# Kernel tuning notes

Measured on AMD Instinct MI355X. Metric: run time of the kernel, lower is better.

## Reference

```python
import jax, jax.numpy as jnp
import numpy as np

CUTOFF = 5.0
N_ATOMS, N_EDGES, D, R = 100000, 1600000, 64, 20


def setup_inputs() -> dict:
    key = jax.random.key(0)
    ks = jax.random.split(key, 12)
    ve = jax.random.normal(ks[0], (N_ATOMS, D, 3), dtype=jnp.float32)
    se = jax.random.normal(ks[1], (N_ATOMS, D), dtype=jnp.float32)
    dirs = jax.random.normal(ks[2], (N_EDGES, 3), dtype=jnp.float32)
    dirs = dirs / jnp.linalg.norm(dirs, axis=-1, keepdims=True)
    dist = jax.random.uniform(ks[3], (N_EDGES,), minval=0.5, maxval=CUTOFF, dtype=jnp.float32)
    nv = dirs * dist[:, None]  # neighbour_vectors with norm in (0.5, cutoff)
    central = jax.random.randint(ks[4], (N_EDGES,), 0, N_ATOMS)
    neigh = jax.random.randint(ks[5], (N_EDGES,), 0, N_ATOMS)
    # Bessel frequencies n*pi/cutoff (learnable in graph-pes)
    freqs = (jnp.arange(1, R + 1, dtype=jnp.float32) * np.pi / CUTOFF)
    W_filter = jax.random.normal(ks[6], (R, 3 * D), dtype=jnp.float32) / np.sqrt(R)
    b_filter = jnp.zeros((3 * D,), dtype=jnp.float32)
    W1 = jax.random.normal(ks[7], (D, D), dtype=jnp.float32) / np.sqrt(D)
    b1 = jnp.zeros((D,), dtype=jnp.float32)
    W2 = jax.random.normal(ks[8], (D, 3 * D), dtype=jnp.float32) / np.sqrt(D)
    b2 = jnp.zeros((3 * D,), dtype=jnp.float32)
    return {
        'vector_embeddings': ve, 'scalar_embeddings': se, 'neighbour_vectors': nv,
        'central_atoms': central, 'neighbours': neigh,
        'freqs': freqs, 'W_filter': W_filter, 'b_filter': b_filter,
        'W1': W1, 'b1': b1, 'W2': W2, 'b2': b2,
    }


def _envelope(d):
    # polynomial envelope, p = 6
    u = d / CUTOFF
    env = 1.0 - 28.0 * u**6 + 48.0 * u**7 - 21.0 * u**8
    return jnp.where(d < CUTOFF, env, 0.0)


def reference(vector_embeddings, scalar_embeddings, neighbour_vectors,
              central_atoms, neighbours, freqs, W_filter, b_filter,
              W1, b1, W2, b2):
    d = jnp.linalg.norm(neighbour_vectors, axis=-1)                 # [E]
    unit = neighbour_vectors / d[:, None]                           # [E, 3]
    # Bessel radial basis: sqrt(2/c) * sin(f_n d) / d
    bessel = np.sqrt(2.0 / CUTOFF) * jnp.sin(freqs[None, :] * d[:, None]) / d[:, None]  # [E, R]
    filt = (bessel @ W_filter + b_filter) * _envelope(d)[:, None]   # [E, 3D]
    # phi: MLP [D, D, 3D] with SiLU between layers
    h = jax.nn.silu(scalar_embeddings @ W1 + b1) @ W2 + b2          # [N, 3D]
    x_ij = filt * h[central_atoms]                                  # [E, 3D]
    a, b, c = jnp.split(x_ij, 3, axis=-1)                           # each [E, D]
    n = scalar_embeddings.shape[0]
    delta_s = jax.ops.segment_sum(a, neighbours, num_segments=n)    # [N, D]
    v_ij = b[:, :, None] * unit[:, None, :] + c[:, :, None] * vector_embeddings[neighbours]  # [E, D, 3]
    delta_v = jax.ops.segment_sum(v_ij, neighbours, num_segments=n)  # [N, D, 3]
    return (delta_v, delta_s)
```

## Files before the change

kernel.cpp:

```cpp
#include <hip/hip_runtime.h>
#include <math.h>

#define DCH 64
#define TD 192
#define RR 20
#define FCUT 5.0f

typedef __attribute__((ext_vector_type(8))) short short8;
typedef __attribute__((ext_vector_type(4))) float f32x4;
typedef __attribute__((ext_vector_type(2))) unsigned int u32x2;

__device__ __forceinline__ unsigned short f2bf(float f) {
    unsigned int u = __float_as_uint(f);
    u += 0x7FFFu + ((u >> 16) & 1u);
    return (unsigned short)(u >> 16);
}
__device__ __forceinline__ float bflo(unsigned int u) {
    return __uint_as_float(u << 16);
}
__device__ __forceinline__ float bfhi(unsigned int u) {
    return __uint_as_float(u & 0xFFFF0000u);
}

__global__ __launch_bounds__(256, 2) void mlp_mfma_kernel(
    const float* __restrict__ se,
    const float* __restrict__ W1, const float* __restrict__ b1,
    const float* __restrict__ W2, const float* __restrict__ b2,
    unsigned short* __restrict__ h2, int N)
{
    const int wid  = threadIdx.x >> 6;
    const int lane = threadIdx.x & 63;
    const int g    = lane >> 4;
    const int c    = lane & 15;

    __shared__ float hmid[4][16][68];
    __shared__ unsigned short hstage[4][16][196];

    short8 W1f[4][2];
    float  b1t[4];
    #pragma unroll
    for (int t = 0; t < 4; ++t) {
        #pragma unroll
        for (int kh = 0; kh < 2; ++kh)
            #pragma unroll
            for (int j = 0; j < 8; ++j) {
                int k = kh * 32 + 8 * g + j;
                W1f[t][kh][j] = (short)f2bf(W1[k * DCH + 16 * t + c]);
            }
        b1t[t] = b1[16 * t + c];
    }
    short8 W2f[12][2];
    float  b2t[12];
    #pragma unroll
    for (int t = 0; t < 12; ++t) {
        #pragma unroll
        for (int kh = 0; kh < 2; ++kh)
            #pragma unroll
            for (int j = 0; j < 8; ++j) {
                int k = kh * 32 + 8 * g + j;
                W2f[t][kh][j] = (short)f2bf(W2[k * TD + 16 * t + c]);
            }
        b2t[t] = b2[16 * t + c];
    }

    for (int base = blockIdx.x * 64; base < N; base += gridDim.x * 64) {
        const int arow = base + wid * 16;
        const int atom = arow + c;
        const bool va  = atom < N;

        const float* sp = se + (size_t)(va ? atom : 0) * DCH;
        short8 A0, A1;
        #pragma unroll
        for (int kh = 0; kh < 2; ++kh) {
            f32x4 q0 = va ? __builtin_nontemporal_load((const f32x4*)(sp + kh*32 + 8*g))
                          : (f32x4){0.f,0.f,0.f,0.f};
            f32x4 q1 = va ? __builtin_nontemporal_load((const f32x4*)(sp + kh*32 + 8*g + 4))
                          : (f32x4){0.f,0.f,0.f,0.f};
            short8& A = kh ? A1 : A0;
            A[0] = (short)f2bf(q0[0]); A[1] = (short)f2bf(q0[1]);
            A[2] = (short)f2bf(q0[2]); A[3] = (short)f2bf(q0[3]);
            A[4] = (short)f2bf(q1[0]); A[5] = (short)f2bf(q1[1]);
            A[6] = (short)f2bf(q1[2]); A[7] = (short)f2bf(q1[3]);
        }

        #pragma unroll
        for (int t = 0; t < 4; ++t) {
            f32x4 C = {0.f, 0.f, 0.f, 0.f};
            C = __builtin_amdgcn_mfma_f32_16x16x32_bf16(A0, W1f[t][0], C, 0, 0, 0);
            C = __builtin_amdgcn_mfma_f32_16x16x32_bf16(A1, W1f[t][1], C, 0, 0, 0);
            #pragma unroll
            for (int reg = 0; reg < 4; ++reg) {
                float x = C[reg] + b1t[t];
                float s = x / (1.0f + __expf(-x));
                hmid[wid][4 * g + reg][16 * t + c] = s;
            }
        }
        __syncthreads();

        short8 B0, B1;
        #pragma unroll
        for (int kh = 0; kh < 2; ++kh) {
            const float* hp = &hmid[wid][c][kh * 32 + 8 * g];
            f32x4 q0 = *(const f32x4*)(hp);
            f32x4 q1 = *(const f32x4*)(hp + 4);
            short8& A = kh ? B1 : B0;
            A[0] = (short)f2bf(q0[0]); A[1] = (short)f2bf(q0[1]);
            A[2] = (short)f2bf(q0[2]); A[3] = (short)f2bf(q0[3]);
            A[4] = (short)f2bf(q1[0]); A[5] = (short)f2bf(q1[1]);
            A[6] = (short)f2bf(q1[2]); A[7] = (short)f2bf(q1[3]);
        }

        #pragma unroll
        for (int t = 0; t < 12; ++t) {
            f32x4 C = {0.f, 0.f, 0.f, 0.f};
            C = __builtin_amdgcn_mfma_f32_16x16x32_bf16(B0, W2f[t][0], C, 0, 0, 0);
            C = __builtin_amdgcn_mfma_f32_16x16x32_bf16(B1, W2f[t][1], C, 0, 0, 0);
            #pragma unroll
            for (int reg = 0; reg < 4; ++reg)
                hstage[wid][4 * g + reg][c * 12 + t] = f2bf(C[reg] + b2t[t]);
        }
        __syncthreads();

        if (lane < 48) {
            #pragma unroll
            for (int i = 0; i < 16; ++i) {
                int a2 = arow + i;
                if (a2 < N)
                    *(u32x2*)((char*)h2 + (size_t)a2 * 384 + lane * 8) =
                        *(const u32x2*)(&hstage[wid][i][lane * 4]);
            }
        }
    }
}

__global__ void hist_kernel(const int* __restrict__ neigh,
                            int* __restrict__ counts, int* __restrict__ pos, int E)
{
    int stride = gridDim.x * blockDim.x;
    for (int e = blockIdx.x * blockDim.x + threadIdx.x; e < E; e += stride) {
        int p = atomicAdd(&counts[neigh[e]], 1);
        __builtin_nontemporal_store(p, &pos[e]);
    }
}

__global__ __launch_bounds__(256) void scan1_kernel(
    const int* __restrict__ counts, int* __restrict__ starts,
    int* __restrict__ bsums, int N)
{
    int tid = threadIdx.x;
    int gid = blockIdx.x * 256 + tid;
    int v = (gid < N) ? counts[gid] : 0;
    int lane = tid & 63, wid = tid >> 6;
    int x = v;
    #pragma unroll
    for (int off = 1; off < 64; off <<= 1) {
        int y = __shfl_up(x, off, 64);
        if (lane >= off) x += y;
    }
    __shared__ int wsum[4];
    if (lane == 63) wsum[wid] = x;
    __syncthreads();
    int add = 0;
    for (int w = 0; w < wid; ++w) add += wsum[w];
    int incl = x + add;
    if (gid < N) starts[gid] = incl - v;
    if (tid == 255) bsums[blockIdx.x] = incl;
}

__global__ __launch_bounds__(512) void scan2_kernel(int* __restrict__ bsums, int M)
{
    int tid = threadIdx.x;
    int v = (tid < M) ? bsums[tid] : 0;
    int lane = tid & 63, wid = tid >> 6;
    int x = v;
    #pragma unroll
    for (int off = 1; off < 64; off <<= 1) {
        int y = __shfl_up(x, off, 64);
        if (lane >= off) x += y;
    }
    __shared__ int wsum[8];
    if (lane == 63) wsum[wid] = x;
    __syncthreads();
    int add = 0;
    for (int w = 0; w < wid; ++w) add += wsum[w];
    int incl = x + add;
    if (tid < M) bsums[tid] = incl - v;
}

__global__ __launch_bounds__(256) void scan3_kernel(
    int* __restrict__ starts, const int* __restrict__ bsums, int N)
{
    int gid = blockIdx.x * 256 + threadIdx.x;
    if (gid < N) starts[gid] += bsums[blockIdx.x];
}

__global__ void fill_kernel(const float* __restrict__ nv, const int* __restrict__ central,
                            const int* __restrict__ neigh, const int* __restrict__ starts,
                            const int* __restrict__ pos, f32x4* __restrict__ payload, int E)
{
    int stride = gridDim.x * blockDim.x;
    for (int e = blockIdx.x * blockDim.x + threadIdx.x; e < E; e += stride) {
        int slot = starts[neigh[e]] + pos[e];
        f32x4 pay;
        pay[0] = __builtin_nontemporal_load(&nv[(size_t)e*3+0]);
        pay[1] = __builtin_nontemporal_load(&nv[(size_t)e*3+1]);
        pay[2] = __builtin_nontemporal_load(&nv[(size_t)e*3+2]);
        pay[3] = __int_as_float(central[e]);
        __builtin_nontemporal_store(pay, &payload[slot]);
    }
}

__global__ __launch_bounds__(256) void gather_kernel(
    const f32x4* __restrict__ payload, const int* __restrict__ starts,
    const int* __restrict__ counts, const unsigned short* __restrict__ h2,
    const float* __restrict__ ve, const float* __restrict__ Wf,
    const float* __restrict__ bfil,
    float* __restrict__ dv, float* __restrict__ ds, int N)
{
    const int wid  = threadIdx.x >> 6;
    const int lane = threadIdx.x & 63;
    const int g    = lane >> 4;
    const int c    = lane & 15;

    short8 Bf[12];
    float  bft[12];
    #pragma unroll
    for (int t = 0; t < 12; ++t) {
        #pragma unroll
        for (int j = 0; j < 8; ++j) {
            int r = 8 * g + j;
            float w = (r < RR) ? Wf[r * TD + 16 * t + c] : 0.0f;
            Bf[t][j] = (short)f2bf(w);
        }
        bft[t] = bfil[16 * t + c];
    }

    const float BC = sqrtf(2.0f / FCUT);
    const float XK = (float)(M_PI / (double)FCUT);
    const char* hb = (const char*)h2;

    for (int atom = blockIdx.x * 4 + wid; atom < N; atom += gridDim.x * 4) {
        const int s   = starts[atom];
        const int cnt = counts[atom];

        float dsa[4] = {0,0,0,0};
        float csm[4] = {0,0,0,0};
        float dvx[4] = {0,0,0,0};
        float dvy[4] = {0,0,0,0};
        float dvz[4] = {0,0,0,0};

        for (int i0 = 0; i0 < cnt; i0 += 16) {
            const bool valid = (i0 + c) < cnt;
            f32x4 p = valid ? __builtin_nontemporal_load(&payload[s + i0 + c])
                            : (f32x4){1.0f, 0.0f, 0.0f, 0.0f};
            float dist = sqrtf(p[0]*p[0] + p[1]*p[1] + p[2]*p[2]);
            float inv  = 1.0f / dist;
            float xa   = dist * XK;

            float u  = dist * (1.0f / FCUT);
            float u2 = u * u;
            float u6 = u2 * u2 * u2;
            float env = 1.0f + u6 * (-28.0f + u * (48.0f - 21.0f * u));
            env = (dist < FCUT && valid) ? env : 0.0f;
            float scale = BC * inv * env;

            float ux = p[0] * inv, uy = p[1] * inv, uz = p[2] * inv;
            int   ca  = valid ? __float_as_int(p[3]) : 0;
            int   hof = ca * 384;

            float bas[8];
            bas[0] = __sinf((float)(8 * g + 1) * xa);
            bas[1] = __sinf((float)(8 * g + 2) * xa);
            float twoc = 2.0f * __cosf(xa);
            #pragma unroll
            for (int j = 2; j < 8; ++j)
                bas[j] = fmaf(twoc, bas[j-1], -bas[j-2]);

            short8 A;
            #pragma unroll
            for (int j = 0; j < 8; ++j)
                A[j] = (short)f2bf(bas[j] * scale);

            float env_r[4], ux_r[4], uy_r[4], uz_r[4];
            int   hof_r[4];
            #pragma unroll
            for (int reg = 0; reg < 4; ++reg) {
                int src = 4 * g + reg;
                env_r[reg] = __shfl(env, src, 64);
                ux_r[reg]  = __shfl(ux,  src, 64);
                uy_r[reg]  = __shfl(uy,  src, 64);
                uz_r[reg]  = __shfl(uz,  src, 64);
                hof_r[reg] = __shfl(hof, src, 64);
            }

            u32x2 hq[4][3];
            #pragma unroll
            for (int reg = 0; reg < 4; ++reg) {
                const char* rp = hb + (size_t)(unsigned)hof_r[reg] + c * 24;
                hq[reg][0] = *(const u32x2*)(rp);
                hq[reg][1] = *(const u32x2*)(rp + 8);
                hq[reg][2] = *(const u32x2*)(rp + 16);
            }

            #pragma unroll
            for (int t = 0; t < 12; ++t) {
                f32x4 C = __builtin_amdgcn_mfma_f32_16x16x32_bf16(
                    A, Bf[t], (f32x4){0.f,0.f,0.f,0.f}, 0, 0, 0);
                #pragma unroll
                for (int reg = 0; reg < 4; ++reg) {
                    unsigned int w = hq[reg][t >> 2][(t >> 1) & 1];
                    float hv = (t & 1) ? bfhi(w) : bflo(w);
                    float filt = fmaf(bft[t], env_r[reg], C[reg]);
                    if (t < 4) {
                        dsa[t] = fmaf(filt, hv, dsa[t]);
                    } else if (t < 8) {
                        float bh = filt * hv;
                        dvx[t-4] = fmaf(bh, ux_r[reg], dvx[t-4]);
                        dvy[t-4] = fmaf(bh, uy_r[reg], dvy[t-4]);
                        dvz[t-4] = fmaf(bh, uz_r[reg], dvz[t-4]);
                    } else {
                        csm[t-8] = fmaf(filt, hv, csm[t-8]);
                    }
                }
            }
        }

        #pragma unroll
        for (int t = 0; t < 4; ++t) {
            dsa[t] += __shfl_xor(dsa[t], 16, 64); dsa[t] += __shfl_xor(dsa[t], 32, 64);
            csm[t] += __shfl_xor(csm[t], 16, 64); csm[t] += __shfl_xor(csm[t], 32, 64);
            dvx[t] += __shfl_xor(dvx[t], 16, 64); dvx[t] += __shfl_xor(dvx[t], 32, 64);
            dvy[t] += __shfl_xor(dvy[t], 16, 64); dvy[t] += __shfl_xor(dvy[t], 32, 64);
            dvz[t] += __shfl_xor(dvz[t], 16, 64); dvz[t] += __shfl_xor(dvz[t], 32, 64);
        }

        float dssel = (g==0) ? dsa[0] : (g==1) ? dsa[1] : (g==2) ? dsa[2] : dsa[3];
        float cssel = (g==0) ? csm[0] : (g==1) ? csm[1] : (g==2) ? csm[2] : csm[3];
        float vxsel = (g==0) ? dvx[0] : (g==1) ? dvx[1] : (g==2) ? dvx[2] : dvx[3];
        float vysel = (g==0) ? dvy[0] : (g==1) ? dvy[1] : (g==2) ? dvy[2] : dvy[3];
        float vzsel = (g==0) ? dvz[0] : (g==1) ? dvz[1] : (g==2) ? dvz[2] : dvz[3];

        int ch = 16 * g + c;
        size_t vb = (size_t)atom * TD + (size_t)ch * 3;
        float v0 = __builtin_nontemporal_load(&ve[vb + 0]);
        float v1 = __builtin_nontemporal_load(&ve[vb + 1]);
        float v2 = __builtin_nontemporal_load(&ve[vb + 2]);
        __builtin_nontemporal_store(fmaf(cssel, v0, vxsel), &dv[vb + 0]);
        __builtin_nontemporal_store(fmaf(cssel, v1, vysel), &dv[vb + 1]);
        __builtin_nontemporal_store(fmaf(cssel, v2, vzsel), &dv[vb + 2]);
        __builtin_nontemporal_store(dssel, &ds[(size_t)atom * DCH + ch]);
    }
}

extern "C" void kernel_launch(void* const* d_in, const int* in_sizes, int n_in,
                              void* d_out, int out_size, void* d_ws, size_t ws_size,
                              hipStream_t stream) {
    const float* ve      = (const float*)d_in[0];
    const float* se      = (const float*)d_in[1];
    const float* nv      = (const float*)d_in[2];
    const int*   central = (const int*)  d_in[3];
    const int*   neigh   = (const int*)  d_in[4];
    const float* Wf      = (const float*)d_in[6];
    const float* bfil    = (const float*)d_in[7];
    const float* W1      = (const float*)d_in[8];
    const float* b1      = (const float*)d_in[9];
    const float* W2      = (const float*)d_in[10];
    const float* b2      = (const float*)d_in[11];

    const int N = in_sizes[1] / DCH;
    const int E = in_sizes[3];

    float* out = (float*)d_out;
    float* dv  = out;
    float* ds  = out + (size_t)N * TD;

    char* wsb = (char*)d_ws;
    size_t off = 0;
    auto wsalloc = [&](size_t bytes) -> void* {
        void* p = wsb + off;
        off = (off + bytes + 255) & ~(size_t)255;
        return p;
    };
    unsigned short* h2      = (unsigned short*)wsalloc((size_t)N * 192 * 2);
    int*            counts  = (int*)   wsalloc((size_t)N * 4);
    int*            starts  = (int*)   wsalloc((size_t)N * 4);
    int*            pos     = (int*)   wsalloc((size_t)E * 4);
    f32x4*          payload = (f32x4*) wsalloc((size_t)E * 16);
    int*            bsums   = (int*)   wsalloc(4096);

    const int nb1 = (N + 255) / 256;
    const int nbm = (N + 63) / 64;

    mlp_mfma_kernel<<<nbm, 256, 0, stream>>>(se, W1, b1, W2, b2, h2, N);

    hipMemsetAsync(counts, 0, (size_t)N * 4, stream);
    hist_kernel<<<2048, 256, 0, stream>>>(neigh, counts, pos, E);
    scan1_kernel<<<nb1, 256, 0, stream>>>(counts, starts, bsums, N);
    scan2_kernel<<<1, 512, 0, stream>>>(bsums, nb1);
    scan3_kernel<<<nb1, 256, 0, stream>>>(starts, bsums, N);
    fill_kernel<<<2048, 256, 0, stream>>>(nv, central, neigh, starts, pos, payload, E);
    gather_kernel<<<2048, 256, 0, stream>>>(payload, starts, counts, h2, ve,
                                            Wf, bfil, dv, ds, N);
}
```

Baseline: 354.0 us.

## Use atomic cursor fill, fold filter bias into MFMA, prefetch payload

The histogram no longer writes per-edge positions. The fill step now takes slots with atomicAdd on a copy of the start offsets, which removes the E-sized pos array and its write and read traffic. In the gather kernel, the filter bias times the envelope is folded into the MFMA as an extra basis row (row 20 holds the bias, A gets env). The next payload chunk is software-prefetched, and the h rows are gathered right after loading central indices instead of through shuffles. In exchange, the fill kernel uses more atomics, the bias is rounded to bf16, and each lane makes extra redundant payload loads to get the central indices.

```diff
diff --git a/kernel.cpp b/kernel.cpp
--- a/kernel.cpp
+++ b/kernel.cpp
@@ -134,13 +134,11 @@
 }
 
 __global__ void hist_kernel(const int* __restrict__ neigh,
-                            int* __restrict__ counts, int* __restrict__ pos, int E)
+                            int* __restrict__ counts, int E)
 {
     int stride = gridDim.x * blockDim.x;
-    for (int e = blockIdx.x * blockDim.x + threadIdx.x; e < E; e += stride) {
-        int p = atomicAdd(&counts[neigh[e]], 1);
-        __builtin_nontemporal_store(p, &pos[e]);
-    }
+    for (int e = blockIdx.x * blockDim.x + threadIdx.x; e < E; e += stride)
+        atomicAdd(&counts[neigh[e]], 1);
 }
 
 __global__ __launch_bounds__(256) void scan1_kernel(
@@ -188,19 +186,24 @@
 }
 
 __global__ __launch_bounds__(256) void scan3_kernel(
-    int* __restrict__ starts, const int* __restrict__ bsums, int N)
+    int* __restrict__ starts, int* __restrict__ starts2,
+    const int* __restrict__ bsums, int N)
 {
     int gid = blockIdx.x * 256 + threadIdx.x;
-    if (gid < N) starts[gid] += bsums[blockIdx.x];
+    if (gid < N) {
+        int v = starts[gid] + bsums[blockIdx.x];
+        starts[gid]  = v;
+        starts2[gid] = v;
+    }
 }
 
 __global__ void fill_kernel(const float* __restrict__ nv, const int* __restrict__ central,
-                            const int* __restrict__ neigh, const int* __restrict__ starts,
-                            const int* __restrict__ pos, f32x4* __restrict__ payload, int E)
+                            const int* __restrict__ neigh, int* __restrict__ starts2,
+                            f32x4* __restrict__ payload, int E)
 {
     int stride = gridDim.x * blockDim.x;
     for (int e = blockIdx.x * blockDim.x + threadIdx.x; e < E; e += stride) {
-        int slot = starts[neigh[e]] + pos[e];
+        int slot = atomicAdd(&starts2[neigh[e]], 1);
         f32x4 pay;
         pay[0] = __builtin_nontemporal_load(&nv[(size_t)e*3+0]);
         pay[1] = __builtin_nontemporal_load(&nv[(size_t)e*3+1]);
@@ -223,16 +226,15 @@
     const int c    = lane & 15;
 
     short8 Bf[12];
-    float  bft[12];
     #pragma unroll
     for (int t = 0; t < 12; ++t) {
         #pragma unroll
         for (int j = 0; j < 8; ++j) {
             int r = 8 * g + j;
-            float w = (r < RR) ? Wf[r * TD + 16 * t + c] : 0.0f;
+            float w = (r < RR) ? Wf[r * TD + 16 * t + c]
+                               : (r == RR ? bfil[16 * t + c] : 0.0f);
             Bf[t][j] = (short)f2bf(w);
         }
-        bft[t] = bfil[16 * t + c];
     }
 
     const float BC = sqrtf(2.0f / FCUT);
@@ -249,11 +251,28 @@
         float dvy[4] = {0,0,0,0};
         float dvz[4] = {0,0,0,0};
 
+        f32x4 p_cur;
+        if (cnt > 0)
+            p_cur = payload[s + min(c, cnt - 1)];
+
         for (int i0 = 0; i0 < cnt; i0 += 16) {
+            f32x4 p_nxt = p_cur;
+            if (i0 + 16 < cnt)
+                p_nxt = payload[s + min(i0 + 16 + c, cnt - 1)];
+
+            u32x2 hq[4][3];
+            #pragma unroll
+            for (int reg = 0; reg < 4; ++reg) {
+                int row = i0 + 4 * g + reg;
+                int ca  = __float_as_int(payload[s + min(row, cnt - 1)][3]);
+                const char* rp = hb + (size_t)(unsigned)(ca * 384) + c * 24;
+                hq[reg][0] = *(const u32x2*)(rp);
+                hq[reg][1] = *(const u32x2*)(rp + 8);
+                hq[reg][2] = *(const u32x2*)(rp + 16);
+            }
+
             const bool valid = (i0 + c) < cnt;
-            f32x4 p = valid ? __builtin_nontemporal_load(&payload[s + i0 + c])
-                            : (f32x4){1.0f, 0.0f, 0.0f, 0.0f};
-            float dist = sqrtf(p[0]*p[0] + p[1]*p[1] + p[2]*p[2]);
+            float dist = sqrtf(p_cur[0]*p_cur[0] + p_cur[1]*p_cur[1] + p_cur[2]*p_cur[2]);
             float inv  = 1.0f / dist;
             float xa   = dist * XK;
 
@@ -264,9 +283,7 @@
             env = (dist < FCUT && valid) ? env : 0.0f;
             float scale = BC * inv * env;
 
-            float ux = p[0] * inv, uy = p[1] * inv, uz = p[2] * inv;
-            int   ca  = valid ? __float_as_int(p[3]) : 0;
-            int   hof = ca * 384;
+            float ux = p_cur[0] * inv, uy = p_cur[1] * inv, uz = p_cur[2] * inv;
 
             float bas[8];
             bas[0] = __sinf((float)(8 * g + 1) * xa);
@@ -280,26 +297,15 @@
             #pragma unroll
             for (int j = 0; j < 8; ++j)
                 A[j] = (short)f2bf(bas[j] * scale);
-
-            float env_r[4], ux_r[4], uy_r[4], uz_r[4];
-            int   hof_r[4];
+            if (g == 2) A[4] = (short)f2bf(env);
+
+            float ux_r[4], uy_r[4], uz_r[4];
             #pragma unroll
             for (int reg = 0; reg < 4; ++reg) {
                 int src = 4 * g + reg;
-                env_r[reg] = __shfl(env, src, 64);
-                ux_r[reg]  = __shfl(ux,  src, 64);
-                uy_r[reg]  = __shfl(uy,  src, 64);
-                uz_r[reg]  = __shfl(uz,  src, 64);
-                hof_r[reg] = __shfl(hof, src, 64);
-            }
-
-            u32x2 hq[4][3];
-            #pragma unroll
-            for (int reg = 0; reg < 4; ++reg) {
-                const char* rp = hb + (size_t)(unsigned)hof_r[reg] + c * 24;
-                hq[reg][0] = *(const u32x2*)(rp);
-                hq[reg][1] = *(const u32x2*)(rp + 8);
-                hq[reg][2] = *(const u32x2*)(rp + 16);
+                ux_r[reg] = __shfl(ux, src, 64);
+                uy_r[reg] = __shfl(uy, src, 64);
+                uz_r[reg] = __shfl(uz, src, 64);
             }
 
             #pragma unroll
@@ -310,19 +316,19 @@
                 for (int reg = 0; reg < 4; ++reg) {
                     unsigned int w = hq[reg][t >> 2][(t >> 1) & 1];
                     float hv = (t & 1) ? bfhi(w) : bflo(w);
-                    float filt = fmaf(bft[t], env_r[reg], C[reg]);
                     if (t < 4) {
-                        dsa[t] = fmaf(filt, hv, dsa[t]);
+                        dsa[t] = fmaf(C[reg], hv, dsa[t]);
                     } else if (t < 8) {
-                        float bh = filt * hv;
+                        float bh = C[reg] * hv;
                         dvx[t-4] = fmaf(bh, ux_r[reg], dvx[t-4]);
                         dvy[t-4] = fmaf(bh, uy_r[reg], dvy[t-4]);
                         dvz[t-4] = fmaf(bh, uz_r[reg], dvz[t-4]);
                     } else {
-                        csm[t-8] = fmaf(filt, hv, csm[t-8]);
+                        csm[t-8] = fmaf(C[reg], hv, csm[t-8]);
                     }
                 }
             }
+            p_cur = p_nxt;
         }
 
         #pragma unroll
@@ -384,7 +390,7 @@
     unsigned short* h2      = (unsigned short*)wsalloc((size_t)N * 192 * 2);
     int*            counts  = (int*)   wsalloc((size_t)N * 4);
     int*            starts  = (int*)   wsalloc((size_t)N * 4);
-    int*            pos     = (int*)   wsalloc((size_t)E * 4);
+    int*            starts2 = (int*)   wsalloc((size_t)N * 4);
     f32x4*          payload = (f32x4*) wsalloc((size_t)E * 16);
     int*            bsums   = (int*)   wsalloc(4096);
 
@@ -394,11 +400,11 @@
     mlp_mfma_kernel<<<nbm, 256, 0, stream>>>(se, W1, b1, W2, b2, h2, N);
 
     hipMemsetAsync(counts, 0, (size_t)N * 4, stream);
-    hist_kernel<<<2048, 256, 0, stream>>>(neigh, counts, pos, E);
+    hist_kernel<<<2048, 256, 0, stream>>>(neigh, counts, E);
     scan1_kernel<<<nb1, 256, 0, stream>>>(counts, starts, bsums, N);
     scan2_kernel<<<1, 512, 0, stream>>>(bsums, nb1);
-    scan3_kernel<<<nb1, 256, 0, stream>>>(starts, bsums, N);
-    fill_kernel<<<2048, 256, 0, stream>>>(nv, central, neigh, starts, pos, payload, E);
+    scan3_kernel<<<nb1, 256, 0, stream>>>(starts, starts2, bsums, N);
+    fill_kernel<<<2048, 256, 0, stream>>>(nv, central, neigh, starts2, payload, E);
     gather_kernel<<<2048, 256, 0, stream>>>(payload, starts, counts, h2, ve,
                                             Wf, bfil, dv, ds, N);
 }
```

Result: slower. 429.1 us (+21.2%).

## Fuse MLP and histogram into one launch and fold scan offsets into consumers

Applied to the files above, without the earlier changes.

The atom MLP and the edge histogram now run in one kernel: the first HIST_BLOCKS blocks do the atomic counting and the rest each compute one 64-atom tile of the MLP, so the two independent stages overlap and one launch goes away. The scan3 pass is removed, and fill and gather add the per-256-block prefix from bsums themselves. In exchange, MLP blocks reload and convert the weights from global memory per tile instead of keeping them in registers across a persistent loop, and the 2-blocks-per-CU launch bound is dropped.

```diff
diff --git a/kernel.cpp b/kernel.cpp
--- a/kernel.cpp
+++ b/kernel.cpp
@@ -5,6 +5,7 @@
 #define TD 192
 #define RR 20
 #define FCUT 5.0f
+#define HIST_BLOCKS 512
 
 typedef __attribute__((ext_vector_type(8))) short short8;
 typedef __attribute__((ext_vector_type(4))) float f32x4;
@@ -22,12 +23,23 @@
     return __uint_as_float(u & 0xFFFF0000u);
 }
 
-__global__ __launch_bounds__(256, 2) void mlp_mfma_kernel(
+__global__ __launch_bounds__(256) void mlp_hist_kernel(
     const float* __restrict__ se,
     const float* __restrict__ W1, const float* __restrict__ b1,
     const float* __restrict__ W2, const float* __restrict__ b2,
-    unsigned short* __restrict__ h2, int N)
-{
+    unsigned short* __restrict__ h2, int N,
+    const int* __restrict__ neigh, int* __restrict__ counts,
+    int* __restrict__ pos, int E)
+{
+    if (blockIdx.x < HIST_BLOCKS) {
+        int stride = HIST_BLOCKS * 256;
+        for (int e = blockIdx.x * 256 + threadIdx.x; e < E; e += stride) {
+            int p = atomicAdd(&counts[neigh[e]], 1);
+            __builtin_nontemporal_store(p, &pos[e]);
+        }
+        return;
+    }
+
     const int wid  = threadIdx.x >> 6;
     const int lane = threadIdx.x & 63;
     const int g    = lane >> 4;
@@ -36,110 +48,86 @@
     __shared__ float hmid[4][16][68];
     __shared__ unsigned short hstage[4][16][196];
 
-    short8 W1f[4][2];
-    float  b1t[4];
+    const int base = (blockIdx.x - HIST_BLOCKS) * 64;
+    const int arow = base + wid * 16;
+    const int atom = arow + c;
+    const bool va  = atom < N;
+
+    const float* sp = se + (size_t)(va ? atom : 0) * DCH;
+    short8 A0, A1;
+    #pragma unroll
+    for (int kh = 0; kh < 2; ++kh) {
+        f32x4 q0 = va ? __builtin_nontemporal_load((const f32x4*)(sp + kh*32 + 8*g))
+                      : (f32x4){0.f,0.f,0.f,0.f};
+        f32x4 q1 = va ? __builtin_nontemporal_load((const f32x4*)(sp + kh*32 + 8*g + 4))
+                      : (f32x4){0.f,0.f,0.f,0.f};
+        short8& A = kh ? A1 : A0;
+        A[0] = (short)f2bf(q0[0]); A[1] = (short)f2bf(q0[1]);
+        A[2] = (short)f2bf(q0[2]); A[3] = (short)f2bf(q0[3]);
+        A[4] = (short)f2bf(q1[0]); A[5] = (short)f2bf(q1[1]);
+        A[6] = (short)f2bf(q1[2]); A[7] = (short)f2bf(q1[3]);
+    }
+
     #pragma unroll
     for (int t = 0; t < 4; ++t) {
-        #pragma unroll
-        for (int kh = 0; kh < 2; ++kh)
-            #pragma unroll
-            for (int j = 0; j < 8; ++j) {
-                int k = kh * 32 + 8 * g + j;
-                W1f[t][kh][j] = (short)f2bf(W1[k * DCH + 16 * t + c]);
-            }
-        b1t[t] = b1[16 * t + c];
-    }
-    short8 W2f[12][2];
-    float  b2t[12];
+        short8 w0, w1;
+        #pragma unroll
+        for (int j = 0; j < 8; ++j) {
+            w0[j] = (short)f2bf(W1[(8 * g + j) * DCH + 16 * t + c]);
+            w1[j] = (short)f2bf(W1[(32 + 8 * g + j) * DCH + 16 * t + c]);
+        }
+        f32x4 C = {0.f, 0.f, 0.f, 0.f};
+        C = __builtin_amdgcn_mfma_f32_16x16x32_bf16(A0, w0, C, 0, 0, 0);
+        C = __builtin_amdgcn_mfma_f32_16x16x32_bf16(A1, w1, C, 0, 0, 0);
+        float bb = b1[16 * t + c];
+        #pragma unroll
+        for (int reg = 0; reg < 4; ++reg) {
+            float x = C[reg] + bb;
+            float s = x / (1.0f + __expf(-x));
+            hmid[wid][4 * g + reg][16 * t + c] = s;
+        }
+    }
+    __syncthreads();
+
+    short8 B0, B1;
+    #pragma unroll
+    for (int kh = 0; kh < 2; ++kh) {
+        const float* hp = &hmid[wid][c][kh * 32 + 8 * g];
+        f32x4 q0 = *(const f32x4*)(hp);
+        f32x4 q1 = *(const f32x4*)(hp + 4);
+        short8& A = kh ? B1 : B0;
+        A[0] = (short)f2bf(q0[0]); A[1] = (short)f2bf(q0[1]);
+        A[2] = (short)f2bf(q0[2]); A[3] = (short)f2bf(q0[3]);
+        A[4] = (short)f2bf(q1[0]); A[5] = (short)f2bf(q1[1]);
+        A[6] = (short)f2bf(q1[2]); A[7] = (short)f2bf(q1[3]);
+    }
+
     #pragma unroll
     for (int t = 0; t < 12; ++t) {
-        #pragma unroll
-        for (int kh = 0; kh < 2; ++kh)
-            #pragma unroll
-            for (int j = 0; j < 8; ++j) {
-                int k = kh * 32 + 8 * g + j;
-                W2f[t][kh][j] = (short)f2bf(W2[k * TD + 16 * t + c]);
-            }
-        b2t[t] = b2[16 * t + c];
-    }
-
-    for (int base = blockIdx.x * 64; base < N; base += gridDim.x * 64) {
-        const int arow = base + wid * 16;
-        const int atom = arow + c;
-        const bool va  = atom < N;
-
-        const float* sp = se + (size_t)(va ? atom : 0) * DCH;
-        short8 A0, A1;
-        #pragma unroll
-        for (int kh = 0; kh < 2; ++kh) {
-            f32x4 q0 = va ? __builtin_nontemporal_load((const f32x4*)(sp + kh*32 + 8*g))
-                          : (f32x4){0.f,0.f,0.f,0.f};
-            f32x4 q1 = va ? __builtin_nontemporal_load((const f32x4*)(sp + kh*32 + 8*g + 4))
-                          : (f32x4){0.f,0.f,0.f,0.f};
-            short8& A = kh ? A1 : A0;
-            A[0] = (short)f2bf(q0[0]); A[1] = (short)f2bf(q0[1]);
-            A[2] = (short)f2bf(q0[2]); A[3] = (short)f2bf(q0[3]);
-            A[4] = (short)f2bf(q1[0]); A[5] = (short)f2bf(q1[1]);
-            A[6] = (short)f2bf(q1[2]); A[7] = (short)f2bf(q1[3]);
-        }
-
-        #pragma unroll
-        for (int t = 0; t < 4; ++t) {
-            f32x4 C = {0.f, 0.f, 0.f, 0.f};
-            C = __builtin_amdgcn_mfma_f32_16x16x32_bf16(A0, W1f[t][0], C, 0, 0, 0);
-            C = __builtin_amdgcn_mfma_f32_16x16x32_bf16(A1, W1f[t][1], C, 0, 0, 0);
-            #pragma unroll
-            for (int reg = 0; reg < 4; ++reg) {
-                float x = C[reg] + b1t[t];
-                float s = x / (1.0f + __expf(-x));
-                hmid[wid][4 * g + reg][16 * t + c] = s;
-            }
-        }
-        __syncthreads();
-
-        short8 B0, B1;
-        #pragma unroll
-        for (int kh = 0; kh < 2; ++kh) {
-            const float* hp = &hmid[wid][c][kh * 32 + 8 * g];
-            f32x4 q0 = *(const f32x4*)(hp);
-            f32x4 q1 = *(const f32x4*)(hp + 4);
-            short8& A = kh ? B1 : B0;
-            A[0] = (short)f2bf(q0[0]); A[1] = (short)f2bf(q0[1]);
-            A[2] = (short)f2bf(q0[2]); A[3] = (short)f2bf(q0[3]);
-            A[4] = (short)f2bf(q1[0]); A[5] = (short)f2bf(q1[1]);
-            A[6] = (short)f2bf(q1[2]); A[7] = (short)f2bf(q1[3]);
-        }
-
-        #pragma unroll
-        for (int t = 0; t < 12; ++t) {
-            f32x4 C = {0.f, 0.f, 0.f, 0.f};
-            C = __builtin_amdgcn_mfma_f32_16x16x32_bf16(B0, W2f[t][0], C, 0, 0, 0);
-            C = __builtin_amdgcn_mfma_f32_16x16x32_bf16(B1, W2f[t][1], C, 0, 0, 0);
-            #pragma unroll
-            for (int reg = 0; reg < 4; ++reg)
-                hstage[wid][4 * g + reg][c * 12 + t] = f2bf(C[reg] + b2t[t]);
-        }
-        __syncthreads();
-
-        if (lane < 48) {
-            #pragma unroll
-            for (int i = 0; i < 16; ++i) {
-                int a2 = arow + i;
-                if (a2 < N)
-                    *(u32x2*)((char*)h2 + (size_t)a2 * 384 + lane * 8) =
-                        *(const u32x2*)(&hstage[wid][i][lane * 4]);
-            }
-        }
-    }
-}
-
-__global__ void hist_kernel(const int* __restrict__ neigh,
-                            int* __restrict__ counts, int* __restrict__ pos, int E)
-{
-    int stride = gridDim.x * blockDim.x;
-    for (int e = blockIdx.x * blockDim.x + threadIdx.x; e < E; e += stride) {
-        int p = atomicAdd(&counts[neigh[e]], 1);
-        __builtin_nontemporal_store(p, &pos[e]);
+        short8 w0, w1;
+        #pragma unroll
+        for (int j = 0; j < 8; ++j) {
+            w0[j] = (short)f2bf(W2[(8 * g + j) * TD + 16 * t + c]);
+            w1[j] = (short)f2bf(W2[(32 + 8 * g + j) * TD + 16 * t + c]);
+        }
+        f32x4 C = {0.f, 0.f, 0.f, 0.f};
+        C = __builtin_amdgcn_mfma_f32_16x16x32_bf16(B0, w0, C, 0, 0, 0);
+        C = __builtin_amdgcn_mfma_f32_16x16x32_bf16(B1, w1, C, 0, 0, 0);
+        float bb = b2[16 * t + c];
+        #pragma unroll
+        for (int reg = 0; reg < 4; ++reg)
+            hstage[wid][4 * g + reg][c * 12 + t] = f2bf(C[reg] + bb);
+    }
+    __syncthreads();
+
+    if (lane < 48) {
+        #pragma unroll
+        for (int i = 0; i < 16; ++i) {
+            int a2 = arow + i;
+            if (a2 < N)
+                *(u32x2*)((char*)h2 + (size_t)a2 * 384 + lane * 8) =
+                    *(const u32x2*)(&hstage[wid][i][lane * 4]);
+        }
     }
 }
 
@@ -187,20 +175,15 @@
     if (tid < M) bsums[tid] = incl - v;
 }
 
-__global__ __launch_bounds__(256) void scan3_kernel(
-    int* __restrict__ starts, const int* __restrict__ bsums, int N)
-{
-    int gid = blockIdx.x * 256 + threadIdx.x;
-    if (gid < N) starts[gid] += bsums[blockIdx.x];
-}
-
 __global__ void fill_kernel(const float* __restrict__ nv, const int* __restrict__ central,
                             const int* __restrict__ neigh, const int* __restrict__ starts,
-                            const int* __restrict__ pos, f32x4* __restrict__ payload, int E)
+                            const int* __restrict__ bsums, const int* __restrict__ pos,
+                            f32x4* __restrict__ payload, int E)
 {
     int stride = gridDim.x * blockDim.x;
     for (int e = blockIdx.x * blockDim.x + threadIdx.x; e < E; e += stride) {
-        int slot = starts[neigh[e]] + pos[e];
+        int na = neigh[e];
+        int slot = starts[na] + bsums[na >> 8] + pos[e];
         f32x4 pay;
         pay[0] = __builtin_nontemporal_load(&nv[(size_t)e*3+0]);
         pay[1] = __builtin_nontemporal_load(&nv[(size_t)e*3+1]);
@@ -212,7 +195,8 @@
 
 __global__ __launch_bounds__(256) void gather_kernel(
     const f32x4* __restrict__ payload, const int* __restrict__ starts,
-    const int* __restrict__ counts, const unsigned short* __restrict__ h2,
+    const int* __restrict__ bsums, const int* __restrict__ counts,
+    const unsigned short* __restrict__ h2,
     const float* __restrict__ ve, const float* __restrict__ Wf,
     const float* __restrict__ bfil,
     float* __restrict__ dv, float* __restrict__ ds, int N)
@@ -240,7 +224,7 @@
     const char* hb = (const char*)h2;
 
     for (int atom = blockIdx.x * 4 + wid; atom < N; atom += gridDim.x * 4) {
-        const int s   = starts[atom];
+        const int s   = starts[atom] + bsums[atom >> 8];
         const int cnt = counts[atom];
 
         float dsa[4] = {0,0,0,0};
@@ -391,14 +375,13 @@
     const int nb1 = (N + 255) / 256;
     const int nbm = (N + 63) / 64;
 
-    mlp_mfma_kernel<<<nbm, 256, 0, stream>>>(se, W1, b1, W2, b2, h2, N);
-
     hipMemsetAsync(counts, 0, (size_t)N * 4, stream);
-    hist_kernel<<<2048, 256, 0, stream>>>(neigh, counts, pos, E);
+    mlp_hist_kernel<<<HIST_BLOCKS + nbm, 256, 0, stream>>>(
+        se, W1, b1, W2, b2, h2, N, neigh, counts, pos, E);
     scan1_kernel<<<nb1, 256, 0, stream>>>(counts, starts, bsums, N);
     scan2_kernel<<<1, 512, 0, stream>>>(bsums, nb1);
-    scan3_kernel<<<nb1, 256, 0, stream>>>(starts, bsums, N);
-    fill_kernel<<<2048, 256, 0, stream>>>(nv, central, neigh, starts, pos, payload, E);
-    gather_kernel<<<2048, 256, 0, stream>>>(payload, starts, counts, h2, ve,
+    fill_kernel<<<2048, 256, 0, stream>>>(nv, central, neigh, starts, bsums, pos,
+                                          payload, E);
+    gather_kernel<<<2048, 256, 0, stream>>>(payload, starts, bsums, counts, h2, ve,
                                             Wf, bfil, dv, ds, N);
 }
```

New measurement: 349.5 us. No clear change (-1.2%).
